# Kernel tuning notes

Hardware: AMD Instinct MI355X
Metric: run time of the kernel (lower is better)

The kernel has to match this reference:

```python
import jax, jax.numpy as jnp
import numpy as np

NEG_SLOPE = 0.2

def _gat_layer(x, src, dst, W, a_s, a_d, b, concat):
    # x: [N, F_in], W: [F_in, H*C], a_s/a_d: [H, C]
    N = x.shape[0]
    H, C = a_s.shape
    h = (x @ W).reshape(N, H, C)                       # per-head projection
    al_s = jnp.sum(h * a_s, axis=-1)                   # [N, H]
    al_d = jnp.sum(h * a_d, axis=-1)                   # [N, H]
    e = jax.nn.leaky_relu(al_s[src] + al_d[dst], NEG_SLOPE)  # [E, H]
    # segment softmax over incoming edges of each dst node
    m = jax.ops.segment_max(e, dst, num_segments=N)    # [N, H]
    ex = jnp.exp(e - m[dst])
    denom = jax.ops.segment_sum(ex, dst, num_segments=N)
    alpha = ex / denom[dst]                            # [E, H]
    msg = h[src] * alpha[:, :, None]                   # [E, H, C]
    out = jax.ops.segment_sum(msg, dst, num_segments=N)  # [N, H, C]
    if concat:
        return out.reshape(N, H * C) + b
    return out.mean(axis=1) + b


def setup_inputs() -> dict:
    key = jax.random.key(0)
    ks = jax.random.split(key, 12)
    N, F_in, H, C1, LAT, E = 16384, 512, 4, 128, 64, 262144
    x = jax.random.normal(ks[0], (N, F_in), dtype=jnp.float32)
    edge_index = jax.random.randint(ks[1], (2, E), 0, N, dtype=jnp.int64)
    s = 0.05
    return {
        'x': x,
        'edge_index': edge_index,
        'W1': jax.random.normal(ks[2], (F_in, H * C1), dtype=jnp.float32) * s,
        'a_src1': jax.random.normal(ks[3], (H, C1), dtype=jnp.float32) * s,
        'a_dst1': jax.random.normal(ks[4], (H, C1), dtype=jnp.float32) * s,
        'b1': jax.random.normal(ks[5], (H * C1,), dtype=jnp.float32) * s,
        'W2': jax.random.normal(ks[6], (H * C1, H * LAT), dtype=jnp.float32) * s,
        'a_src2': jax.random.normal(ks[7], (H, LAT), dtype=jnp.float32) * s,
        'a_dst2': jax.random.normal(ks[8], (H, LAT), dtype=jnp.float32) * s,
        'b2': jax.random.normal(ks[9], (LAT,), dtype=jnp.float32) * s,
    }


def reference(x, edge_index, W1, a_src1, a_dst1, b1, W2, a_src2, a_dst2, b2):
    N = x.shape[0]
    # PyG GATConv default add_self_loops=True
    loop = jnp.arange(N, dtype=edge_index.dtype)
    src = jnp.concatenate([edge_index[0], loop])
    dst = jnp.concatenate([edge_index[1], loop])
    h = jax.nn.relu(_gat_layer(x, src, dst, W1, a_src1, a_dst1, b1, concat=True))
    out = _gat_layer(h, src, dst, W2, a_src2, a_dst2, b2, concat=False)
    return out
```

## Files before the change

### kernel.cpp

```cpp
#include <hip/hip_runtime.h>
#include <stdint.h>
#include <stddef.h>
#include <limits.h>

typedef __bf16 bf16;
typedef __bf16 bf16x4 __attribute__((ext_vector_type(4)));
typedef __bf16 bf16x8 __attribute__((ext_vector_type(8)));
typedef float  f32x4  __attribute__((ext_vector_type(4)));

#define CAP 128

static __device__ __forceinline__ float lrelu(float x) { return x > 0.f ? x : 0.2f * x; }
static __device__ __forceinline__ float san(float v) { return (fabsf(v) < 1e4f) ? v : 0.0f; }
static __device__ __forceinline__ float wexp(float e) { return __expf(fminf(e, 30.f)); }

static __device__ __forceinline__ void async_load16(const bf16* g, bf16* l) {
  __builtin_amdgcn_global_load_lds((const __attribute__((address_space(1))) void*)g,
                                   (__attribute__((address_space(3))) void*)l, 16, 0, 0);
}

static __device__ __forceinline__ void drain_barrier() {
  asm volatile("s_waitcnt vmcnt(0) lgkmcnt(0)" ::: "memory");
  __builtin_amdgcn_s_barrier();
}


__global__ __launch_bounds__(256) void prep_w(int* __restrict__ cnt,
                                              const float* __restrict__ W1,
                                              const float* __restrict__ W2,
                                              bf16* __restrict__ W1T,
                                              bf16* __restrict__ W2T,
                                              int N) {
  int b = blockIdx.x;
  if (b < N / 256) { cnt[b * 256 + threadIdx.x] = 0; return; }
  b -= N / 256;
  __shared__ bf16 t[32][33];
  const float* in; bf16* out; int R, C, bx, by;
  if (b < 256) { in = W1; out = W1T; R = 512; C = 512; by = b >> 4; bx = b & 15; }
  else         { b -= 256; in = W2; out = W2T; R = 512; C = 256; by = b >> 3; bx = b & 7; }
  const int lane = threadIdx.x & 31, r8 = threadIdx.x >> 5;
#pragma unroll
  for (int k = 0; k < 4; ++k) {
    int r = by * 32 + r8 + k * 8, c = bx * 32 + lane;
    t[lane][r8 + k * 8] = (bf16)san(in[(size_t)r * C + c]);
  }
  __syncthreads();
#pragma unroll
  for (int k = 0; k < 4; ++k) {
    int oc = bx * 32 + r8 + k * 8;
    out[(size_t)oc * R + by * 32 + lane] = t[r8 + k * 8][lane];
  }
}


__global__ __launch_bounds__(256) void gemm_al_l1(const float* __restrict__ X,
                                                  const bf16* __restrict__ BT,
                                                  bf16* __restrict__ C,
                                                  const float* __restrict__ a_s,
                                                  const float* __restrict__ a_d,
                                                  float* __restrict__ al_s,
                                                  float* __restrict__ al_d,
                                                  const int* __restrict__ src,
                                                  const int* __restrict__ dst,
                                                  int E, int* __restrict__ cnt,
                                                  int* __restrict__ slots,
                                                  int M, int N, int K) {
  __shared__ __align__(16) bf16 As[2][64 * 32];
  __shared__ __align__(16) bf16 Bs[2][128 * 32];
  __shared__ float alred[2][64][2];
  const int tid = threadIdx.x;
  const int b   = blockIdx.x;

  if (b >= 1024) {
    for (int e = (b - 1024) * 256 + tid; e < E; e += 512 * 256) {
      int d = dst[e];
      int pos = atomicAdd(&cnt[d], 1);
      if (pos < CAP) slots[(size_t)d * CAP + pos] = src[e];
    }
    return;
  }

  const int lane = tid & 63;
  const int wave = tid >> 6;
  const int m0 = (b & 255) * 64;
  const int head = b >> 8;
  const int n0 = head * 128;
  const int wm = (wave >> 1) * 32;
  const int wn = (wave & 1) * 64;

  f32x4 acc[2][4] = {};

  const int id1 = tid + 256;
  const float* apx = X  + (size_t)(m0 + (tid >> 2)) * K + (tid & 3) * 8;
  const bf16*  b0p = BT + (size_t)(n0 + (tid >> 2)) * K + (tid & 3) * 8;
  const bf16*  b1p = BT + (size_t)(n0 + (id1 >> 2)) * K + (id1 & 3) * 8;

  const int kq = (lane >> 4) * 8;
  const int rA = wm + (lane & 15);
  const int rB = wn + (lane & 15);

  {
    f32x4 u0 = *(const f32x4*)(apx);
    f32x4 u1 = *(const f32x4*)(apx + 4);
    async_load16(b0p, &Bs[0][tid * 8]);
    async_load16(b1p, &Bs[0][id1 * 8]);
    bf16x8 w;
#pragma unroll
    for (int k = 0; k < 4; ++k) { w[k] = (bf16)san(u0[k]); w[4 + k] = (bf16)san(u1[k]); }
    *(bf16x8*)&As[0][tid * 8] = w;
    drain_barrier();
  }

  int cur = 0;
  for (int k0 = 0; k0 < K; k0 += 32) {
    const int kn = (k0 + 32 < K) ? (k0 + 32) : k0;
    f32x4 u0 = *(const f32x4*)(apx + kn);
    f32x4 u1 = *(const f32x4*)(apx + kn + 4);
    async_load16(b0p + kn, &Bs[cur ^ 1][tid * 8]);
    async_load16(b1p + kn, &Bs[cur ^ 1][id1 * 8]);

    bf16x8 af[2], bfv[4];
#pragma unroll
    for (int i = 0; i < 2; ++i) af[i]  = *(const bf16x8*)&As[cur][(rA + i * 16) * 32 + kq];
#pragma unroll
    for (int j = 0; j < 4; ++j) bfv[j] = *(const bf16x8*)&Bs[cur][(rB + j * 16) * 32 + kq];
#pragma unroll
    for (int i = 0; i < 2; ++i)
#pragma unroll
      for (int j = 0; j < 4; ++j)
        acc[i][j] = __builtin_amdgcn_mfma_f32_16x16x32_bf16(af[i], bfv[j], acc[i][j], 0, 0, 0);

    bf16x8 w;
#pragma unroll
    for (int k = 0; k < 4; ++k) { w[k] = (bf16)san(u0[k]); w[4 + k] = (bf16)san(u1[k]); }
    *(bf16x8*)&As[cur ^ 1][tid * 8] = w;

    drain_barrier();
    cur ^= 1;
  }

  const int cc = lane & 15;
  const int rb = (lane >> 4) * 4;
#pragma unroll
  for (int i = 0; i < 2; ++i)
#pragma unroll
    for (int j = 0; j < 4; ++j) {
      int gcol = n0 + wn + j * 16 + cc;
#pragma unroll
      for (int r = 0; r < 4; ++r) {
        int grow = m0 + wm + i * 16 + rb + r;
        C[(size_t)grow * N + gcol] = (bf16)acc[i][j][r];
      }
    }

  {
    float asv[4], adv[4];
#pragma unroll
    for (int j = 0; j < 4; ++j) {
      int col = head * 128 + wn + j * 16 + cc;
      asv[j] = san(a_s[col]);
      adv[j] = san(a_d[col]);
    }
    const int wnh = wn >> 6;
#pragma unroll
    for (int i = 0; i < 2; ++i)
#pragma unroll
      for (int r = 0; r < 4; ++r) {
        float ps = 0.f, pd = 0.f;
#pragma unroll
        for (int j = 0; j < 4; ++j) { ps += acc[i][j][r] * asv[j]; pd += acc[i][j][r] * adv[j]; }
#pragma unroll
        for (int off = 1; off <= 8; off <<= 1) {
          ps += __shfl_xor(ps, off);
          pd += __shfl_xor(pd, off);
        }
        if (cc == 0) {
          int row = wm + i * 16 + rb + r;
          alred[wnh][row][0] = ps;
          alred[wnh][row][1] = pd;
        }
      }
    __syncthreads();
    if (tid < 64) {
      al_s[(size_t)(m0 + tid) * 4 + head] = alred[0][tid][0] + alred[1][tid][0];
      al_d[(size_t)(m0 + tid) * 4 + head] = alred[0][tid][1] + alred[1][tid][1];
    }
  }
}


__global__ __launch_bounds__(256) void gemm_al_l2(const bf16* __restrict__ A,
                                                  const bf16* __restrict__ BT,
                                                  bf16* __restrict__ C,
                                                  const float* __restrict__ a_s,
                                                  const float* __restrict__ a_d,
                                                  float* __restrict__ al_s,
                                                  float* __restrict__ al_d,
                                                  int M, int N, int K) {
  __shared__ __align__(16) bf16 As[2][64 * 32];
  __shared__ __align__(16) bf16 Bs[2][64 * 32];
  __shared__ float alred[2][64][2];
  const int tid  = threadIdx.x;
  const int lane = tid & 63;
  const int wave = tid >> 6;
  const int m0   = blockIdx.x * 64;
  const int head = blockIdx.y;
  const int n0   = head * 64;
  const int wm = (wave >> 1) * 32;
  const int wn = (wave & 1) * 32;

  f32x4 acc[2][2] = {};

  const bf16* ap = A  + (size_t)(m0 + (tid >> 2)) * K + (tid & 3) * 8;
  const bf16* bp = BT + (size_t)(n0 + (tid >> 2)) * K + (tid & 3) * 8;

  const int kq = (lane >> 4) * 8;
  const int rA = wm + (lane & 15);
  const int rB = wn + (lane & 15);

  async_load16(ap, &As[0][tid * 8]);
  async_load16(bp, &Bs[0][tid * 8]);
  drain_barrier();

  int cur = 0;
  for (int k0 = 0; k0 < K; k0 += 32) {
    const int kn = (k0 + 32 < K) ? (k0 + 32) : k0;
    async_load16(ap + kn, &As[cur ^ 1][tid * 8]);
    async_load16(bp + kn, &Bs[cur ^ 1][tid * 8]);

    bf16x8 af[2], bfv[2];
#pragma unroll
    for (int i = 0; i < 2; ++i) af[i]  = *(const bf16x8*)&As[cur][(rA + i * 16) * 32 + kq];
#pragma unroll
    for (int j = 0; j < 2; ++j) bfv[j] = *(const bf16x8*)&Bs[cur][(rB + j * 16) * 32 + kq];
#pragma unroll
    for (int i = 0; i < 2; ++i)
#pragma unroll
      for (int j = 0; j < 2; ++j)
        acc[i][j] = __builtin_amdgcn_mfma_f32_16x16x32_bf16(af[i], bfv[j], acc[i][j], 0, 0, 0);

    drain_barrier();
    cur ^= 1;
  }

  const int cc = lane & 15;
  const int rb = (lane >> 4) * 4;
#pragma unroll
  for (int i = 0; i < 2; ++i)
#pragma unroll
    for (int j = 0; j < 2; ++j) {
      int gcol = n0 + wn + j * 16 + cc;
#pragma unroll
      for (int r = 0; r < 4; ++r) {
        int grow = m0 + wm + i * 16 + rb + r;
        C[(size_t)grow * N + gcol] = (bf16)acc[i][j][r];
      }
    }

  {
    float asv[2], adv[2];
#pragma unroll
    for (int j = 0; j < 2; ++j) {
      int col = n0 + wn + j * 16 + cc;
      asv[j] = san(a_s[col]);
      adv[j] = san(a_d[col]);
    }
    const int wnh = wn >> 5;
#pragma unroll
    for (int i = 0; i < 2; ++i)
#pragma unroll
      for (int r = 0; r < 4; ++r) {
        float ps = 0.f, pd = 0.f;
#pragma unroll
        for (int j = 0; j < 2; ++j) { ps += acc[i][j][r] * asv[j]; pd += acc[i][j][r] * adv[j]; }
#pragma unroll
        for (int off = 1; off <= 8; off <<= 1) {
          ps += __shfl_xor(ps, off);
          pd += __shfl_xor(pd, off);
        }
        if (cc == 0) {
          int row = wm + i * 16 + rb + r;
          alred[wnh][row][0] = ps;
          alred[wnh][row][1] = pd;
        }
      }
    __syncthreads();
    if (tid < 64) {
      al_s[(size_t)(m0 + tid) * 4 + head] = alred[0][tid][0] + alred[1][tid][0];
      al_d[(size_t)(m0 + tid) * 4 + head] = alred[0][tid][1] + alred[1][tid][1];
    }
  }
}


__global__ __launch_bounds__(256) void aggregate1_f(const bf16* __restrict__ h1,
                                                    const float* __restrict__ al_s,
                                                    const float* __restrict__ al_d,
                                                    const int* __restrict__ cnt,
                                                    int* __restrict__ slots,
                                                    const float* __restrict__ bias,
                                                    bf16* __restrict__ out) {
  __shared__ int   sIdx[4][64];
  __shared__ f32x4 sW[4][64];
  const int wv   = threadIdx.x >> 6;
  const int lane = threadIdx.x & 63;
  const int n = blockIdx.x * 4 + wv;
  const int cb = lane * 8;
  const int hd = lane >> 4;
  const int beg = n * CAP;
  const int len = min(cnt[n], CAP);
  const f32x4 alsn = *(const f32x4*)(al_s + (size_t)n * 4);
  const f32x4 aldn = *(const f32x4*)(al_d + (size_t)n * 4);

  const float wself = wexp(lrelu(alsn[hd] + aldn[hd]));
  bf16x8 hv0 = *(const bf16x8*)(h1 + (size_t)n * 512 + cb);
  float acc[8];
#pragma unroll
  for (int k = 0; k < 8; ++k) acc[k] = wself * (float)hv0[k];

  f32x4 Lv = {0.f, 0.f, 0.f, 0.f};
  if (lane == 0) {
#pragma unroll
    for (int h = 0; h < 4; ++h) Lv[h] = wexp(lrelu(alsn[h] + aldn[h]));
  }

  if (len <= 64) {
    int v = (lane < len) ? slots[beg + lane] : INT_MAX;
    if (len > 1) {
#pragma unroll
      for (int k = 2; k <= 64; k <<= 1) {
#pragma unroll
        for (int j = k >> 1; j > 0; j >>= 1) {
          int p = __shfl_xor(v, j);
          bool take_min = (((lane & k) == 0) == ((lane & j) == 0));
          v = take_min ? min(v, p) : max(v, p);
        }
      }
      if (lane < len) slots[beg + lane] = v;
    }
    if (lane < len) {
      sIdx[wv][lane] = v;
      f32x4 a = *(const f32x4*)(al_s + (size_t)v * 4);
      f32x4 w;
#pragma unroll
      for (int h = 0; h < 4; ++h) w[h] = wexp(lrelu(a[h] + aldn[h]));
      sW[wv][lane] = w;
#pragma unroll
      for (int h = 0; h < 4; ++h) Lv[h] += w[h];
    }
    for (int j0 = 0; j0 < len; j0 += 8) {
      bf16x8 rv[8];
      float  wt[8];
#pragma unroll
      for (int t = 0; t < 8; ++t) {
        int jj = j0 + t;
        int s  = sIdx[wv][jj < len ? jj : len - 1];
        rv[t]  = *(const bf16x8*)(h1 + (size_t)s * 512 + cb);
        wt[t]  = (jj < len) ? sW[wv][jj][hd] : 0.f;
      }
#pragma unroll
      for (int t = 0; t < 8; ++t)
#pragma unroll
        for (int k = 0; k < 8; ++k) acc[k] += wt[t] * (float)rv[t][k];
    }
  } else {
    if (lane == 0) {
      for (int i = beg + 1; i < beg + len; ++i) {
        int v = slots[i];
        int j = i - 1;
        while (j >= beg && slots[j] > v) { slots[j + 1] = slots[j]; --j; }
        slots[j + 1] = v;
      }
    }
    asm volatile("s_waitcnt vmcnt(0)" ::: "memory");
    for (int c0 = beg; c0 < beg + len; c0 += 64) {
      const int cl = min(64, beg + len - c0);
      if (lane < cl) {
        int s = slots[c0 + lane];
        sIdx[wv][lane] = s;
        f32x4 a = *(const f32x4*)(al_s + (size_t)s * 4);
        f32x4 w;
#pragma unroll
        for (int h = 0; h < 4; ++h) w[h] = wexp(lrelu(a[h] + aldn[h]));
        sW[wv][lane] = w;
#pragma unroll
        for (int h = 0; h < 4; ++h) Lv[h] += w[h];
      }
      for (int j0 = 0; j0 < cl; j0 += 8) {
        bf16x8 rv[8];
        float  wt[8];
#pragma unroll
        for (int t = 0; t < 8; ++t) {
          int jj = j0 + t;
          int s  = sIdx[wv][jj < cl ? jj : cl - 1];
          rv[t]  = *(const bf16x8*)(h1 + (size_t)s * 512 + cb);
          wt[t]  = (jj < cl) ? sW[wv][jj][hd] : 0.f;
        }
#pragma unroll
        for (int t = 0; t < 8; ++t)
#pragma unroll
          for (int k = 0; k < 8; ++k) acc[k] += wt[t] * (float)rv[t][k];
      }
    }
  }

  for (int off = 32; off; off >>= 1) {
#pragma unroll
    for (int h = 0; h < 4; ++h) Lv[h] += __shfl_xor(Lv[h], off);
  }
  const float inv = 1.0f / Lv[hd];
  bf16x8 ov;
#pragma unroll
  for (int k = 0; k < 8; ++k)
    ov[k] = (bf16)fmaxf(acc[k] * inv + san(bias[cb + k]), 0.f);
  *(bf16x8*)(out + (size_t)n * 512 + cb) = ov;
}


__global__ __launch_bounds__(256) void aggregate2_f(const bf16* __restrict__ h2,
                                                    const float* __restrict__ al_s,
                                                    const float* __restrict__ al_d,
                                                    const int* __restrict__ cnt,
                                                    const int* __restrict__ slots,
                                                    const float* __restrict__ bias,
                                                    float* __restrict__ out) {
  __shared__ int   sIdx[4][64];
  __shared__ f32x4 sW[4][64];
  const int wv   = threadIdx.x >> 6;
  const int lane = threadIdx.x & 63;
  const int n = blockIdx.x * 4 + wv;
  const int hd = lane >> 4;
  const int cb = lane * 4;
  const int beg = n * CAP;
  const int len = min(cnt[n], CAP);
  const f32x4 alsn = *(const f32x4*)(al_s + (size_t)n * 4);
  const f32x4 aldn = *(const f32x4*)(al_d + (size_t)n * 4);

  const float wself = wexp(lrelu(alsn[hd] + aldn[hd]));
  bf16x4 hv0 = *(const bf16x4*)(h2 + (size_t)n * 256 + cb);
  float acc0 = wself * (float)hv0[0], acc1 = wself * (float)hv0[1];
  float acc2 = wself * (float)hv0[2], acc3 = wself * (float)hv0[3];
  f32x4 Lv = {0.f, 0.f, 0.f, 0.f};
  if (lane == 0) {
#pragma unroll
    for (int h = 0; h < 4; ++h) Lv[h] = wexp(lrelu(alsn[h] + aldn[h]));
  }
  for (int c0 = beg; c0 < beg + len; c0 += 64) {
    const int cl = min(64, beg + len - c0);
    if (lane < cl) {
      int s = slots[c0 + lane];
      sIdx[wv][lane] = s;
      f32x4 a = *(const f32x4*)(al_s + (size_t)s * 4);
      f32x4 w;
#pragma unroll
      for (int h = 0; h < 4; ++h) w[h] = wexp(lrelu(a[h] + aldn[h]));
      sW[wv][lane] = w;
#pragma unroll
      for (int h = 0; h < 4; ++h) Lv[h] += w[h];
    }
    for (int j0 = 0; j0 < cl; j0 += 8) {
      bf16x4 rv[8];
      float  wt[8];
#pragma unroll
      for (int t = 0; t < 8; ++t) {
        int jj = j0 + t;
        int s  = sIdx[wv][jj < cl ? jj : cl - 1];
        rv[t]  = *(const bf16x4*)(h2 + (size_t)s * 256 + cb);
        wt[t]  = (jj < cl) ? sW[wv][jj][hd] : 0.f;
      }
#pragma unroll
      for (int t = 0; t < 8; ++t) {
        acc0 += wt[t] * (float)rv[t][0];
        acc1 += wt[t] * (float)rv[t][1];
        acc2 += wt[t] * (float)rv[t][2];
        acc3 += wt[t] * (float)rv[t][3];
      }
    }
  }
  for (int off = 32; off; off >>= 1) {
#pragma unroll
    for (int h = 0; h < 4; ++h) Lv[h] += __shfl_xor(Lv[h], off);
  }
  const float inv = 1.0f / Lv[hd];
  acc0 *= inv; acc1 *= inv; acc2 *= inv; acc3 *= inv;
  acc0 += __shfl_xor(acc0, 16); acc1 += __shfl_xor(acc1, 16);
  acc2 += __shfl_xor(acc2, 16); acc3 += __shfl_xor(acc3, 16);
  acc0 += __shfl_xor(acc0, 32); acc1 += __shfl_xor(acc1, 32);
  acc2 += __shfl_xor(acc2, 32); acc3 += __shfl_xor(acc3, 32);
  if (lane < 16) {
    int ob = lane * 4;
    f32x4 ov;
    ov[0] = 0.25f * acc0 + san(bias[ob]);
    ov[1] = 0.25f * acc1 + san(bias[ob + 1]);
    ov[2] = 0.25f * acc2 + san(bias[ob + 2]);
    ov[3] = 0.25f * acc3 + san(bias[ob + 3]);
    *(f32x4*)(out + (size_t)n * 64 + ob) = ov;
  }
}


extern "C" void kernel_launch(void* const* d_in, const int* in_sizes, int n_in,
                              void* d_out, int out_size, void* d_ws, size_t ws_size,
                              hipStream_t stream) {
  const float* x   = (const float*)d_in[0];
  const int*   ei  = (const int*)d_in[1];
  const float* W1  = (const float*)d_in[2];
  const float* as1 = (const float*)d_in[3];
  const float* ad1 = (const float*)d_in[4];
  const float* b1  = (const float*)d_in[5];
  const float* W2  = (const float*)d_in[6];
  const float* as2 = (const float*)d_in[7];
  const float* ad2 = (const float*)d_in[8];
  const float* b2  = (const float*)d_in[9];
  float* outp = (float*)d_out;

  const int N = in_sizes[0] / 512;
  const int E = in_sizes[1] / 2;
  const int* src = ei;
  const int* dst = ei + E;

  char* p = (char*)d_ws;
  auto alloc = [&](size_t bytes) {
    char* r = p;
    p += (bytes + 255) & ~(size_t)255;
    return r;
  };
  bf16* h1    = (bf16*)alloc((size_t)N * 512 * 2);
  bf16* hbuf  = (bf16*)alloc((size_t)N * 512 * 2);
  bf16* W1T   = (bf16*)alloc((size_t)512 * 512 * 2);
  bf16* W2T   = (bf16*)alloc((size_t)256 * 512 * 2);
  float* al_s1 = (float*)alloc((size_t)N * 4 * 4);
  float* al_d1 = (float*)alloc((size_t)N * 4 * 4);
  float* al_s2 = (float*)alloc((size_t)N * 4 * 4);
  float* al_d2 = (float*)alloc((size_t)N * 4 * 4);
  int* cnt     = (int*)alloc((size_t)N * 4);
  int* slots   = (int*)alloc((size_t)N * CAP * 4);
  bf16* h2 = h1;

  prep_w<<<N / 256 + 256 + 128, 256, 0, stream>>>(cnt, W1, W2, W1T, W2T, N);

  gemm_al_l1<<<1024 + 512, 256, 0, stream>>>(x, W1T, h1, as1, ad1, al_s1, al_d1,
                                             src, dst, E, cnt, slots, N, 512, 512);
  aggregate1_f<<<N / 4, 256, 0, stream>>>(h1, al_s1, al_d1, cnt, slots, b1, hbuf);

  gemm_al_l2<<<dim3(N / 64, 4), 256, 0, stream>>>(hbuf, W2T, h2, as2, ad2, al_s2, al_d2,
                                                  N, 256, 512);
  aggregate2_f<<<N / 4, 256, 0, stream>>>(h2, al_s2, al_d2, cnt, slots, b2, outp);
}
```

Before: 193.6 us.

## Split layer-1 aggregation into sort/normalizer pass and column-sliced gather kernel

The fused layer-1 aggregation kernel is split in two. A new pass sorts each node's neighbor slots and writes the inverse softmax denominators per head. A second kernel launches eight blocks per node group, each covering a 64-column slice, with eight sub-groups of lanes gathering different neighbors in parallel and combining them through shuffle reductions. The aim is more memory-level parallelism and occupancy in the gather, at the cost of an extra launch, recomputed edge weights, and more slot and al_s reads across the slice blocks.

Result: slower. 215.0 us (+11.1%).

```diff
diff --git a/kernel.cpp b/kernel.cpp
--- a/kernel.cpp
+++ b/kernel.cpp
@@ -293,35 +293,23 @@
 }
 
 
-__global__ __launch_bounds__(256) void aggregate1_f(const bf16* __restrict__ h1,
-                                                    const float* __restrict__ al_s,
-                                                    const float* __restrict__ al_d,
-                                                    const int* __restrict__ cnt,
-                                                    int* __restrict__ slots,
-                                                    const float* __restrict__ bias,
-                                                    bf16* __restrict__ out) {
-  __shared__ int   sIdx[4][64];
-  __shared__ f32x4 sW[4][64];
+__global__ __launch_bounds__(256) void sort_mkL(const float* __restrict__ al_s,
+                                                const float* __restrict__ al_d,
+                                                const int* __restrict__ cnt,
+                                                int* __restrict__ slots,
+                                                float* __restrict__ Linv) {
   const int wv   = threadIdx.x >> 6;
   const int lane = threadIdx.x & 63;
   const int n = blockIdx.x * 4 + wv;
-  const int cb = lane * 8;
-  const int hd = lane >> 4;
   const int beg = n * CAP;
   const int len = min(cnt[n], CAP);
   const f32x4 alsn = *(const f32x4*)(al_s + (size_t)n * 4);
   const f32x4 aldn = *(const f32x4*)(al_d + (size_t)n * 4);
 
-  const float wself = wexp(lrelu(alsn[hd] + aldn[hd]));
-  bf16x8 hv0 = *(const bf16x8*)(h1 + (size_t)n * 512 + cb);
-  float acc[8];
-#pragma unroll
-  for (int k = 0; k < 8; ++k) acc[k] = wself * (float)hv0[k];
-
-  f32x4 Lv = {0.f, 0.f, 0.f, 0.f};
+  f32x4 L = {0.f, 0.f, 0.f, 0.f};
   if (lane == 0) {
 #pragma unroll
-    for (int h = 0; h < 4; ++h) Lv[h] = wexp(lrelu(alsn[h] + aldn[h]));
+    for (int h = 0; h < 4; ++h) L[h] = wexp(lrelu(alsn[h] + aldn[h]));
   }
 
   if (len <= 64) {
@@ -339,29 +327,9 @@
       if (lane < len) slots[beg + lane] = v;
     }
     if (lane < len) {
-      sIdx[wv][lane] = v;
       f32x4 a = *(const f32x4*)(al_s + (size_t)v * 4);
-      f32x4 w;
-#pragma unroll
-      for (int h = 0; h < 4; ++h) w[h] = wexp(lrelu(a[h] + aldn[h]));
-      sW[wv][lane] = w;
-#pragma unroll
-      for (int h = 0; h < 4; ++h) Lv[h] += w[h];
-    }
-    for (int j0 = 0; j0 < len; j0 += 8) {
-      bf16x8 rv[8];
-      float  wt[8];
-#pragma unroll
-      for (int t = 0; t < 8; ++t) {
-        int jj = j0 + t;
-        int s  = sIdx[wv][jj < len ? jj : len - 1];
-        rv[t]  = *(const bf16x8*)(h1 + (size_t)s * 512 + cb);
-        wt[t]  = (jj < len) ? sW[wv][jj][hd] : 0.f;
-      }
-#pragma unroll
-      for (int t = 0; t < 8; ++t)
-#pragma unroll
-        for (int k = 0; k < 8; ++k) acc[k] += wt[t] * (float)rv[t][k];
+#pragma unroll
+      for (int h = 0; h < 4; ++h) L[h] += wexp(lrelu(a[h] + aldn[h]));
     }
   } else {
     if (lane == 0) {
@@ -377,43 +345,83 @@
       const int cl = min(64, beg + len - c0);
       if (lane < cl) {
         int s = slots[c0 + lane];
-        sIdx[wv][lane] = s;
         f32x4 a = *(const f32x4*)(al_s + (size_t)s * 4);
-        f32x4 w;
-#pragma unroll
-        for (int h = 0; h < 4; ++h) w[h] = wexp(lrelu(a[h] + aldn[h]));
-        sW[wv][lane] = w;
-#pragma unroll
-        for (int h = 0; h < 4; ++h) Lv[h] += w[h];
-      }
-      for (int j0 = 0; j0 < cl; j0 += 8) {
-        bf16x8 rv[8];
-        float  wt[8];
-#pragma unroll
-        for (int t = 0; t < 8; ++t) {
-          int jj = j0 + t;
-          int s  = sIdx[wv][jj < cl ? jj : cl - 1];
-          rv[t]  = *(const bf16x8*)(h1 + (size_t)s * 512 + cb);
-          wt[t]  = (jj < cl) ? sW[wv][jj][hd] : 0.f;
-        }
-#pragma unroll
-        for (int t = 0; t < 8; ++t)
-#pragma unroll
-          for (int k = 0; k < 8; ++k) acc[k] += wt[t] * (float)rv[t][k];
+#pragma unroll
+        for (int h = 0; h < 4; ++h) L[h] += wexp(lrelu(a[h] + aldn[h]));
       }
     }
   }
 
   for (int off = 32; off; off >>= 1) {
 #pragma unroll
-    for (int h = 0; h < 4; ++h) Lv[h] += __shfl_xor(Lv[h], off);
-  }
-  const float inv = 1.0f / Lv[hd];
-  bf16x8 ov;
-#pragma unroll
-  for (int k = 0; k < 8; ++k)
-    ov[k] = (bf16)fmaxf(acc[k] * inv + san(bias[cb + k]), 0.f);
-  *(bf16x8*)(out + (size_t)n * 512 + cb) = ov;
+    for (int h = 0; h < 4; ++h) L[h] += __shfl_xor(L[h], off);
+  }
+  if (lane == 0) {
+    f32x4 o;
+#pragma unroll
+    for (int h = 0; h < 4; ++h) o[h] = 1.0f / L[h];
+    *(f32x4*)(Linv + (size_t)n * 4) = o;
+  }
+}
+
+
+__global__ __launch_bounds__(256) void aggregate1_s(const bf16* __restrict__ h1,
+                                                    const float* __restrict__ al_s,
+                                                    const float* __restrict__ al_d,
+                                                    const int* __restrict__ cnt,
+                                                    const int* __restrict__ slots,
+                                                    const float* __restrict__ Linv,
+                                                    const float* __restrict__ bias,
+                                                    bf16* __restrict__ out) {
+  const int sl   = blockIdx.x & 7;
+  const int g    = blockIdx.x >> 3;
+  const int wv   = threadIdx.x >> 6;
+  const int lane = threadIdx.x & 63;
+  const int n    = g * 4 + wv;
+  const int hd   = sl >> 1;
+  const int c8   = lane & 7;
+  const int sub  = lane >> 3;
+  const int cbase = sl * 64 + c8 * 8;
+  const int beg = n * CAP;
+  const int len = min(cnt[n], CAP);
+  const float aldh = al_d[(size_t)n * 4 + hd];
+
+  float acc[8] = {};
+  if (sub == 0) {
+    float wself = wexp(lrelu(al_s[(size_t)n * 4 + hd] + aldh));
+    bf16x8 hv = *(const bf16x8*)(h1 + (size_t)n * 512 + cbase);
+#pragma unroll
+    for (int k = 0; k < 8; ++k) acc[k] = wself * (float)hv[k];
+  }
+
+  for (int c0 = 0; c0 < len; c0 += 64) {
+    const int cl = min(64, len - c0);
+    int v = (lane < cl) ? slots[beg + c0 + lane] : 0;
+    float wl = 0.f;
+    if (lane < cl) wl = wexp(lrelu(al_s[(size_t)v * 4 + hd] + aldh));
+    for (int j0 = 0; j0 < cl; j0 += 8) {
+      int jj = j0 + sub;
+      int   sj = __shfl(v, jj);
+      float wj = __shfl(wl, jj);
+      bf16x8 rv = *(const bf16x8*)(h1 + (size_t)sj * 512 + cbase);
+#pragma unroll
+      for (int k = 0; k < 8; ++k) acc[k] += wj * (float)rv[k];
+    }
+  }
+
+#pragma unroll
+  for (int off = 8; off <= 32; off <<= 1)
+#pragma unroll
+    for (int k = 0; k < 8; ++k) acc[k] += __shfl_xor(acc[k], off);
+
+  if (sub == 0) {
+    const float inv = Linv[(size_t)n * 4 + hd];
+    bf16x8 ov;
+#pragma unroll
+    for (int k = 0; k < 8; ++k)
+      ov[k] = (bf16)fmaxf(acc[k] * inv + san(bias[cbase + k]), 0.f);
+    *(bf16x8*)(out + (size_t)n * 512 + cbase) = ov;
+  }
 }
 
 
@@ -533,6 +541,7 @@
   float* al_d1 = (float*)alloc((size_t)N * 4 * 4);
   float* al_s2 = (float*)alloc((size_t)N * 4 * 4);
   float* al_d2 = (float*)alloc((size_t)N * 4 * 4);
+  float* Linv1 = (float*)alloc((size_t)N * 4 * 4);
   int* cnt     = (int*)alloc((size_t)N * 4);
   int* slots   = (int*)alloc((size_t)N * CAP * 4);
   bf16* h2 = h1;
@@ -541,7 +550,9 @@
 
   gemm_al_l1<<<1024 + 512, 256, 0, stream>>>(x, W1T, h1, as1, ad1, al_s1, al_d1,
                                              src, dst, E, cnt, slots, N, 512, 512);
-  aggregate1_f<<<N / 4, 256, 0, stream>>>(h1, al_s1, al_d1, cnt, slots, b1, hbuf);
+  sort_mkL<<<N / 4, 256, 0, stream>>>(al_s1, al_d1, cnt, slots, Linv1);
+  aggregate1_s<<<8 * (N / 4), 256, 0, stream>>>(h1, al_s1, al_d1, cnt, slots, Linv1,
+                                                b1, hbuf);
 
   gemm_al_l2<<<dim3(N / 64, 4), 256, 0, stream>>>(hbuf, W2T, h2, as2, ad2, al_s2, al_d2,
                                                   N, 256, 512);
```
